# Performance work log

Hardware: AMD Instinct MI355X
Metric: run time of the kernel (lower is better)

The kernel has to match this reference:

```python
import jax, jax.numpy as jnp
import numpy as np

B, S, E, F = 64, 8192, 8, 32  # batch, seq, embed_dim(=n_qubits), ffn_dim


def setup_inputs() -> dict:
    key = jax.random.key(0)
    k_x, k_t, k_w1, k_b1, k_w2, k_b2 = jax.random.split(key, 6)
    x = jax.random.normal(k_x, (B, S, E), dtype=jnp.float32)
    theta = jax.random.normal(k_t, (E,), dtype=jnp.float32)  # trainable RX angles
    lim1 = 1.0 / np.sqrt(E)
    lim2 = 1.0 / np.sqrt(F)
    w1 = jax.random.uniform(k_w1, (E, F), jnp.float32, -lim1, lim1)
    b1 = jax.random.uniform(k_b1, (F,), jnp.float32, -lim1, lim1)
    w2 = jax.random.uniform(k_w2, (F, E), jnp.float32, -lim2, lim2)
    b2 = jax.random.uniform(k_b2, (E,), jnp.float32, -lim2, lim2)
    return {"x": x, "theta": theta, "w1": w1, "b1": b1, "w2": w2, "b2": b2}


def reference(x, theta, w1, b1, w2, b2):
    # Quantum circuit: per wire i, RX(x_i) then RX(theta_i) on |0>, measure PauliZ.
    # Single-qubit RX gates compose: <Z> after RX(phi)|0> = cos(phi). Wires are
    # independent (no entangling gates), so MeasureAll(PauliZ) = cos(x + theta).
    q_out = jnp.cos(x + theta)                      # [B, S, E]
    h = jax.nn.relu(q_out @ w1 + b1)                # [B, S, F]
    return h @ w2 + b2                              # [B, S, E]
```

## Files before the change

### kernel.cpp

```cpp
#include <hip/hip_runtime.h>


#define TPB 256
#define TOKT 2

__global__ __launch_bounds__(TPB, 4) void ffq_kernel(
    const float4* __restrict__ xv,
    const float*  __restrict__ theta,
    const float*  __restrict__ w1,
    const float*  __restrict__ b1,
    const float*  __restrict__ w2,
    const float*  __restrict__ b2,
    float4*       __restrict__ outv,
    int ntok)
{
    const int base   = blockIdx.x * TPB + threadIdx.x;
    const int stride = gridDim.x * TPB;

    float th[8], bb2[8];
#pragma unroll
    for (int e = 0; e < 8; ++e) { th[e] = theta[e]; bb2[e] = b2[e]; }

    float4 a[TOKT], c[TOKT];
#pragma unroll
    for (int t = 0; t < TOKT; ++t) {
        int g = base + t * stride;
        if (g < ntok) {
            a[t] = xv[2 * g];
            c[t] = xv[2 * g + 1];
        } else {
            a[t] = make_float4(0.f, 0.f, 0.f, 0.f);
            c[t] = make_float4(0.f, 0.f, 0.f, 0.f);
        }
    }

    float q[TOKT][8];
    float o[TOKT][8];
#pragma unroll
    for (int t = 0; t < TOKT; ++t) {
        q[t][0] = __cosf(a[t].x + th[0]);
        q[t][1] = __cosf(a[t].y + th[1]);
        q[t][2] = __cosf(a[t].z + th[2]);
        q[t][3] = __cosf(a[t].w + th[3]);
        q[t][4] = __cosf(c[t].x + th[4]);
        q[t][5] = __cosf(c[t].y + th[5]);
        q[t][6] = __cosf(c[t].z + th[6]);
        q[t][7] = __cosf(c[t].w + th[7]);
#pragma unroll
        for (int e = 0; e < 8; ++e) o[t][e] = bb2[e];
    }

#pragma unroll 2
    for (int f = 0; f < 32; ++f) {
        const float bb = b1[f];
        float wa[8], wb[8];
#pragma unroll
        for (int e = 0; e < 8; ++e) wa[e] = w1[e * 32 + f];
#pragma unroll
        for (int e = 0; e < 8; ++e) wb[e] = w2[f * 8 + e];
#pragma unroll
        for (int t = 0; t < TOKT; ++t) {
            float h = bb;
#pragma unroll
            for (int e = 0; e < 8; ++e) h = fmaf(q[t][e], wa[e], h);
            h = fmaxf(h, 0.0f);
#pragma unroll
            for (int e = 0; e < 8; ++e) o[t][e] = fmaf(h, wb[e], o[t][e]);
        }
    }

#pragma unroll
    for (int t = 0; t < TOKT; ++t) {
        int g = base + t * stride;
        if (g < ntok) {
            outv[2 * g]     = make_float4(o[t][0], o[t][1], o[t][2], o[t][3]);
            outv[2 * g + 1] = make_float4(o[t][4], o[t][5], o[t][6], o[t][7]);
        }
    }
}

extern "C" void kernel_launch(void* const* d_in, const int* in_sizes, int n_in,
                              void* d_out, int out_size, void* d_ws, size_t ws_size,
                              hipStream_t stream) {
    const float* x     = (const float*)d_in[0];
    const float* theta = (const float*)d_in[1];
    const float* w1    = (const float*)d_in[2];
    const float* b1    = (const float*)d_in[3];
    const float* w2    = (const float*)d_in[4];
    const float* b2    = (const float*)d_in[5];
    float* out = (float*)d_out;

    const int ntok = in_sizes[0] / 8;
    const int total_threads = (ntok + TOKT - 1) / TOKT;
    const int grid = (total_threads + TPB - 1) / TPB;

    ffq_kernel<<<grid, TPB, 0, stream>>>(
        (const float4*)x, theta, w1, b1, w2, b2, (float4*)out, ntok);
}
```

Baseline: 84.00 us.

## Pack FFN weights into per-f records and software-prefetch next record

A small prep kernel repacks w1 columns, w2 rows and b1 into contiguous 32-float records per hidden unit in the workspace. The main kernel then reads each record with contiguous uniform loads and double-buffers them, loading record f+1 while computing f, to hide scalar load latency. The launch_bounds occupancy hint is also dropped. This adds an extra kernel launch and more live registers, which may lower occupancy.

```diff
diff --git a/kernel.cpp b/kernel.cpp
--- a/kernel.cpp
+++ b/kernel.cpp
@@ -3,14 +3,26 @@
 
 #define TPB 256
 #define TOKT 2
+#define RECS 32
 
-__global__ __launch_bounds__(TPB, 4) void ffq_kernel(
+__global__ void prep_kernel(const float* __restrict__ w1,
+                            const float* __restrict__ b1,
+                            const float* __restrict__ w2,
+                            float* __restrict__ wrec) {
+    int f = threadIdx.x;
+    float* r = wrec + f * RECS;
+#pragma unroll
+    for (int e = 0; e < 8; ++e) r[e]     = w1[e * 32 + f];
+#pragma unroll
+    for (int e = 0; e < 8; ++e) r[8 + e] = w2[f * 8 + e];
+    r[16] = b1[f];
+}
+
+__global__ __launch_bounds__(TPB) void ffq_kernel(
     const float4* __restrict__ xv,
     const float*  __restrict__ theta,
-    const float*  __restrict__ w1,
-    const float*  __restrict__ b1,
-    const float*  __restrict__ w2,
     const float*  __restrict__ b2,
+    const float*  __restrict__ wrec,
     float4*       __restrict__ outv,
     int ntok)
 {
@@ -50,23 +62,36 @@
         for (int e = 0; e < 8; ++e) o[t][e] = bb2[e];
     }
 
+    float cwa[8], cva[8], cb1;
+#pragma unroll
+    for (int i = 0; i < 8; ++i) { cwa[i] = wrec[i]; cva[i] = wrec[8 + i]; }
+    cb1 = wrec[16];
+
 #pragma unroll 2
     for (int f = 0; f < 32; ++f) {
-        const float bb = b1[f];
-        float wa[8], wb[8];
+        float nwa[8], nva[8], nb1;
+        if (f < 31) {
+            const float* nr = wrec + (f + 1) * RECS;
 #pragma unroll
-        for (int e = 0; e < 8; ++e) wa[e] = w1[e * 32 + f];
+            for (int i = 0; i < 8; ++i) { nwa[i] = nr[i]; nva[i] = nr[8 + i]; }
+            nb1 = nr[16];
+        } else {
 #pragma unroll
-        for (int e = 0; e < 8; ++e) wb[e] = w2[f * 8 + e];
+            for (int i = 0; i < 8; ++i) { nwa[i] = 0.f; nva[i] = 0.f; }
+            nb1 = 0.f;
+        }
 #pragma unroll
         for (int t = 0; t < TOKT; ++t) {
-            float h = bb;
+            float h = cb1;
 #pragma unroll
-            for (int e = 0; e < 8; ++e) h = fmaf(q[t][e], wa[e], h);
+            for (int e = 0; e < 8; ++e) h = fmaf(q[t][e], cwa[e], h);
             h = fmaxf(h, 0.0f);
 #pragma unroll
-            for (int e = 0; e < 8; ++e) o[t][e] = fmaf(h, wb[e], o[t][e]);
+            for (int e = 0; e < 8; ++e) o[t][e] = fmaf(h, cva[e], o[t][e]);
         }
+#pragma unroll
+        for (int i = 0; i < 8; ++i) { cwa[i] = nwa[i]; cva[i] = nva[i]; }
+        cb1 = nb1;
     }
 
 #pragma unroll
@@ -88,12 +113,14 @@
     const float* b1    = (const float*)d_in[3];
     const float* w2    = (const float*)d_in[4];
     const float* b2    = (const float*)d_in[5];
-    float* out = (float*)d_out;
+    float* out  = (float*)d_out;
+    float* wrec = (float*)d_ws;
 
     const int ntok = in_sizes[0] / 8;
     const int total_threads = (ntok + TOKT - 1) / TOKT;
     const int grid = (total_threads + TPB - 1) / TPB;
 
+    prep_kernel<<<1, 32, 0, stream>>>(w1, b1, w2, wrec);
     ffq_kernel<<<grid, TPB, 0, stream>>>(
-        (const float4*)x, theta, w1, b1, w2, b2, (float4*)out, ntok);
+        (const float4*)x, theta, b2, wrec, (float4*)out, ntok);
 }
```

Measured after the change: 86.73 us. 3.2% more time.
